# Performance work log

Measured on AMD Instinct MI355X. Metric: run time of the kernel, lower is better.

## Reference

```python
import jax, jax.numpy as jnp
import numpy as np

C, H, W = 3, 224, 224
P = 14  # patches per row
PS = H // P  # 16
PATCH_DIM = C * PS * PS  # 768
HIDDEN = 768


def patchify(images):
    # images: [n, c, h, w] -> [n, P*P, c*PS*PS], flatten order (c, ph, pw)
    n = images.shape[0]
    x = images.reshape(n, C, P, PS, P, PS)
    x = x.transpose(0, 2, 4, 1, 3, 5)  # [n, Pi, Pj, c, ps, ps]
    return x.reshape(n, P * P, PATCH_DIM)


def setup_inputs() -> dict:
    key = jax.random.key(0)
    k1, k2, k3 = jax.random.split(key, 3)
    images = jax.random.normal(k1, (128, C, H, W), dtype=jnp.float32)
    # nn.Linear(patch_embedding_dim, hidden_dim): weight [out, in], bias [out]
    bound = 1.0 / np.sqrt(PATCH_DIM)
    W_lin = jax.random.uniform(k2, (HIDDEN, PATCH_DIM), minval=-bound, maxval=bound, dtype=jnp.float32)
    b_lin = jax.random.uniform(k3, (HIDDEN,), minval=-bound, maxval=bound, dtype=jnp.float32)
    cls_token = jnp.ones((1, HIDDEN), dtype=jnp.float32)
    return {"images": images, "W_lin": W_lin, "b_lin": b_lin, "cls_token": cls_token}


def reference(images, W_lin, b_lin, cls_token):
    patches = patchify(images)                        # [n, 196, 768]
    hidden = jnp.einsum('npd,hd->nph', patches, W_lin) + b_lin  # [n, 196, H]
    n = images.shape[0]
    cls = jnp.broadcast_to(cls_token[None], (n, 1, HIDDEN))
    return jnp.concatenate([cls, hidden], axis=1)     # [n, 197, H]
```

## Files before the change

kernel.cpp:

```cpp
#include <hip/hip_runtime.h>
#include <cstdint>


#define PGRID 14
#define PSZ   16
#define CHN   3
#define IMGW  224
#define KDIM  768
#define NDIM  768
#define NPATCH 196

typedef short bf16x8 __attribute__((ext_vector_type(8)));
typedef short short8v __attribute__((ext_vector_type(8)));
typedef float f32x4  __attribute__((ext_vector_type(4)));

__device__ __forceinline__ short bf16rne(float f) {
    uint32_t u = __builtin_bit_cast(uint32_t, f);
    u += 0x7FFFu + ((u >> 16) & 1u);
    return (short)(u >> 16);
}

__device__ __forceinline__ short8v cvt8(float4 v0, float4 v1) {
    short8v s;
    s[0] = bf16rne(v0.x); s[1] = bf16rne(v0.y); s[2] = bf16rne(v0.z); s[3] = bf16rne(v0.w);
    s[4] = bf16rne(v1.x); s[5] = bf16rne(v1.y); s[6] = bf16rne(v1.z); s[7] = bf16rne(v1.w);
    return s;
}

__device__ __forceinline__ void gload_lds16(const void* g, void* l) {
    __builtin_amdgcn_global_load_lds(
        (const __attribute__((address_space(1))) unsigned int*)g,
        (__attribute__((address_space(3))) unsigned int*)l, 16, 0, 0);
}

__global__ __launch_bounds__(256) void prep_patch(
    const float* __restrict__ img, short* __restrict__ A, int M)
{
    int t = blockIdx.x * 256 + threadIdx.x;
    if (t >= M * 96) return;
    int m  = t / 96;
    int k8 = t - m * 96;
    int k  = k8 * 8;
    int c  = k >> 8;
    int ph = (k >> 4) & 15;
    int pw = k & 15;
    int im = m / NPATCH;
    int p  = m - im * NPATCH;
    int Pi = p / PGRID;
    int Pj = p - Pi * PGRID;
    const float* src = img + (((long)(im * CHN + c) * IMGW + Pi * PSZ + ph) * IMGW + Pj * PSZ + pw);
    float4 v0 = *(const float4*)src;
    float4 v1 = *(const float4*)(src + 4);
    *(short8v*)(A + (long)m * KDIM + k) = cvt8(v0, v1);
}

__global__ __launch_bounds__(256) void prep_small(
    const float* __restrict__ Wl, const float* __restrict__ cls,
    short* __restrict__ Wb, float* __restrict__ out, int n_img)
{
    int t = blockIdx.x * 256 + threadIdx.x;
    const int WCH = KDIM * NDIM / 8;
    if (t < WCH) {
        float4 v0 = *(const float4*)(Wl + (long)t * 8);
        float4 v1 = *(const float4*)(Wl + (long)t * 8 + 4);
        *(short8v*)(Wb + (long)t * 8) = cvt8(v0, v1);
    } else {
        int u = t - WCH;
        if (u < n_img * 96) {
            int im = u / 96;
            int k8 = u - im * 96;
            float4 v0 = *(const float4*)(cls + k8 * 8);
            float4 v1 = *(const float4*)(cls + k8 * 8 + 4);
            float* dst = out + (long)im * 197 * NDIM + k8 * 8;
            *(float4*)dst = v0;
            *(float4*)(dst + 4) = v1;
        }
    }
}

__global__ __launch_bounds__(256) void vit_gemm2(
    const short* __restrict__ A, const short* __restrict__ B,
    const float* __restrict__ bias, float* __restrict__ out, int M)
{
    __shared__ short As[128 * 64];
    __shared__ short Bs[128 * 64];

    const int tid = threadIdx.x;
    const int m0 = blockIdx.y * 128;
    const int n0 = blockIdx.x * 128;
    const int wave = tid >> 6;
    const int lane = tid & 63;

    const int srow = tid >> 3;
    const int sk   = (tid & 7) ^ (srow & 7);
    const long abase = (long)(m0 + srow) * KDIM + sk * 8;
    const long bbase = (long)(n0 + srow) * KDIM + sk * 8;
    char* AsB = (char*)As;
    char* BsB = (char*)Bs;
    const int ldsw = wave * 1024;

    const int wm = (wave & 1) * 64;
    const int wn = (wave >> 1) * 64;
    const int wq = lane >> 4;
    const int lr = lane & 15;
    const int blk0 = ((wq)     ^ (lr & 7)) * 8;
    const int blk1 = ((wq + 4) ^ (lr & 7)) * 8;

    f32x4 acc[4][4] = {};

    for (int kk = 0; kk < KDIM; kk += 64) {
        #pragma unroll
        for (int j = 0; j < 4; ++j) {
            gload_lds16(A + abase + (long)j * 32 * KDIM + kk, AsB + j * 4096 + ldsw);
            gload_lds16(B + bbase + (long)j * 32 * KDIM + kk, BsB + j * 4096 + ldsw);
        }
        __syncthreads();

        #pragma unroll
        for (int ks = 0; ks < 2; ++ks) {
            const int blk = ks ? blk1 : blk0;
            bf16x8 a[4], b[4];
            #pragma unroll
            for (int i = 0; i < 4; ++i)
                a[i] = *(const bf16x8*)(&As[(wm + i * 16 + lr) * 64 + blk]);
            #pragma unroll
            for (int i = 0; i < 4; ++i)
                b[i] = *(const bf16x8*)(&Bs[(wn + i * 16 + lr) * 64 + blk]);
            #pragma unroll
            for (int i = 0; i < 4; ++i)
                #pragma unroll
                for (int j = 0; j < 4; ++j)
                    acc[i][j] = __builtin_amdgcn_mfma_f32_16x16x32_bf16(a[i], b[j], acc[i][j], 0, 0, 0);
        }
        __syncthreads();
    }

    float bv[4];
    #pragma unroll
    for (int j = 0; j < 4; ++j) bv[j] = bias[n0 + wn + j * 16 + lr];

    #pragma unroll
    for (int i = 0; i < 4; ++i) {
        #pragma unroll
        for (int r = 0; r < 4; ++r) {
            int gm = m0 + wm + i * 16 + wq * 4 + r;
            if (gm < M) {
                int im = gm / NPATCH;
                int p  = gm - im * NPATCH;
                long orow = ((long)im * 197 + 1 + p) * (long)NDIM;
                #pragma unroll
                for (int j = 0; j < 4; ++j)
                    out[orow + n0 + wn + j * 16 + lr] = acc[i][j][r] + bv[j];
            }
        }
    }
}

#define LDSTR 40
__global__ __launch_bounds__(256) void vit_gemm_fb(
    const float* __restrict__ img, const float* __restrict__ Wl,
    const float* __restrict__ bias, float* __restrict__ out, int n_img)
{
    const int M = n_img * NPATCH;
    __shared__ short As[128 * LDSTR];
    __shared__ short Bs[128 * LDSTR];
    const int tid = threadIdx.x;
    const int m0 = blockIdx.y * 128;
    const int n0 = blockIdx.x * 128;
    const int col4  = tid & 7;
    const int rbase = tid >> 3;
    long arow[4];
    for (int rr = 0; rr < 4; ++rr) {
        int m = m0 + rbase + rr * 32;
        int mm = (m < M) ? m : (M - 1);
        int im = mm / NPATCH;
        int p  = mm % NPATCH;
        int Pi = p / PGRID;
        int Pj = p % PGRID;
        arow[rr] = ((long)(im * CHN) * IMGW + Pi * PSZ) * IMGW + Pj * PSZ;
    }
    const int lane = tid & 63;
    const int wave = tid >> 6;
    const int wm = (wave & 1) * 64;
    const int wn = (wave >> 1) * 64;
    const int wq = lane >> 4;
    const int lr = lane & 15;
    f32x4 acc[4][4] = {};
    for (int k0 = 0; k0 < KDIM; k0 += 32) {
        {
            int k  = k0 + col4 * 4;
            int c  = k >> 8;
            int ph = (k >> 4) & 15;
            int pw = k & 15;
            long koff = (long)(c * IMGW + ph) * IMGW + pw;
            #pragma unroll
            for (int rr = 0; rr < 4; ++rr) {
                const float4 v = *(const float4*)(img + arow[rr] + koff);
                int row = rbase + rr * 32;
                short4 s;
                s.x = bf16rne(v.x); s.y = bf16rne(v.y);
                s.z = bf16rne(v.z); s.w = bf16rne(v.w);
                *(short4*)(&As[row * LDSTR + col4 * 4]) = s;
            }
        }
        {
            int k = k0 + col4 * 4;
            #pragma unroll
            for (int rr = 0; rr < 4; ++rr) {
                int nrow = rbase + rr * 32;
                const float4 v = *(const float4*)(Wl + (long)(n0 + nrow) * KDIM + k);
                short4 s;
                s.x = bf16rne(v.x); s.y = bf16rne(v.y);
                s.z = bf16rne(v.z); s.w = bf16rne(v.w);
                *(short4*)(&Bs[nrow * LDSTR + col4 * 4]) = s;
            }
        }
        __syncthreads();
        bf16x8 a[4], b[4];
        #pragma unroll
        for (int i = 0; i < 4; ++i)
            a[i] = *(const bf16x8*)(&As[(wm + i * 16 + lr) * LDSTR + wq * 8]);
        #pragma unroll
        for (int i = 0; i < 4; ++i)
            b[i] = *(const bf16x8*)(&Bs[(wn + i * 16 + lr) * LDSTR + wq * 8]);
        #pragma unroll
        for (int i = 0; i < 4; ++i)
            #pragma unroll
            for (int j = 0; j < 4; ++j)
                acc[i][j] = __builtin_amdgcn_mfma_f32_16x16x32_bf16(a[i], b[j], acc[i][j], 0, 0, 0);
        __syncthreads();
    }
    float bv[4];
    #pragma unroll
    for (int j = 0; j < 4; ++j) bv[j] = bias[n0 + wn + j * 16 + lr];
    #pragma unroll
    for (int i = 0; i < 4; ++i) {
        #pragma unroll
        for (int r = 0; r < 4; ++r) {
            int gm = m0 + wm + i * 16 + wq * 4 + r;
            if (gm < M) {
                int im = gm / NPATCH;
                int p  = gm % NPATCH;
                long orow = ((long)im * 197 + 1 + p) * (long)NDIM;
                #pragma unroll
                for (int j = 0; j < 4; ++j)
                    out[orow + n0 + wn + j * 16 + lr] = acc[i][j][r] + bv[j];
            }
        }
    }
}

__global__ __launch_bounds__(256) void cls_fill(
    const float* __restrict__ cls, float* __restrict__ out, int n_img)
{
    int i = blockIdx.x * 256 + threadIdx.x;
    if (i < n_img * NDIM) {
        int im = i / NDIM;
        int n  = i - im * NDIM;
        out[(long)im * 197 * NDIM + n] = cls[n];
    }
}

extern "C" void kernel_launch(void* const* d_in, const int* in_sizes, int n_in,
                              void* d_out, int out_size, void* d_ws, size_t ws_size,
                              hipStream_t stream) {
    const float* img  = (const float*)d_in[0];
    const float* Wl   = (const float*)d_in[1];
    const float* bias = (const float*)d_in[2];
    const float* cls  = (const float*)d_in[3];
    float* out = (float*)d_out;

    int n_img = in_sizes[0] / (CHN * IMGW * IMGW);
    int M = n_img * NPATCH;
    int mblocks = (M + 127) / 128;
    long Mpad = (long)mblocks * 128;

    size_t need = (size_t)(Mpad * KDIM + (long)KDIM * NDIM) * sizeof(short);
    if (ws_size >= need) {
        short* A_ws = (short*)d_ws;
        short* Wb   = A_ws + Mpad * KDIM;

        prep_patch<<<(M * 96 + 255) / 256, 256, 0, stream>>>(img, A_ws, M);
        int small_total = KDIM * NDIM / 8 + n_img * 96;
        prep_small<<<(small_total + 255) / 256, 256, 0, stream>>>(Wl, cls, Wb, out, n_img);

        dim3 grid(NDIM / 128, mblocks);
        vit_gemm2<<<grid, 256, 0, stream>>>(A_ws, Wb, bias, out, M);
    } else {
        dim3 grid(NDIM / 128, mblocks);
        vit_gemm_fb<<<grid, 256, 0, stream>>>(img, Wl, bias, out, n_img);
        int cls_elems = n_img * NDIM;
        cls_fill<<<(cls_elems + 255) / 256, 256, 0, stream>>>(cls, out, n_img);
    }
}
```

Baseline: 193.9 us.

## Register-prefetch GEMM tiles and remap blocks for XCD-local M-tile sharing

Replaces the direct global-to-LDS loads with register staging, so the next K-slice is fetched from global memory while MFMAs run on the current slice in LDS. Also switches to a 1D grid where each XCD (block index mod 8) gets whole M-groups across all six N tiles, aiming to improve L2 reuse of A tiles. This costs extra VGPRs for the prefetch registers and an LDS store pass. The grid is padded to a multiple of 8 groups, and the surplus blocks exit early.

After: 181.4 us. 6.4% less time.

```diff
diff --git a/kernel.cpp b/kernel.cpp
--- a/kernel.cpp
+++ b/kernel.cpp
@@ -25,12 +25,6 @@
     s[0] = bf16rne(v0.x); s[1] = bf16rne(v0.y); s[2] = bf16rne(v0.z); s[3] = bf16rne(v0.w);
     s[4] = bf16rne(v1.x); s[5] = bf16rne(v1.y); s[6] = bf16rne(v1.z); s[7] = bf16rne(v1.w);
     return s;
-}
-
-__device__ __forceinline__ void gload_lds16(const void* g, void* l) {
-    __builtin_amdgcn_global_load_lds(
-        (const __attribute__((address_space(1))) unsigned int*)g,
-        (__attribute__((address_space(3))) unsigned int*)l, 16, 0, 0);
 }
 
 __global__ __launch_bounds__(256) void prep_patch(
@@ -78,16 +72,27 @@
     }
 }
 
-__global__ __launch_bounds__(256) void vit_gemm2(
+__global__ __launch_bounds__(256) void vit_gemm3(
     const short* __restrict__ A, const short* __restrict__ B,
-    const float* __restrict__ bias, float* __restrict__ out, int M)
-{
+    const float* __restrict__ bias, float* __restrict__ out,
+    int M, int mgroups)
+{
+    {
+    }
+    const int bid = blockIdx.x;
+    const int xcd = bid & 7;
+    const int s   = bid >> 3;
+    const int gq  = s / 6;
+    const int j   = s - gq * 6;
+    const int g   = gq * 8 + xcd;
+    if (g >= mgroups) return;
+    const int m0 = g * 128;
+    const int n0 = j * 128;
+
     __shared__ short As[128 * 64];
     __shared__ short Bs[128 * 64];
 
     const int tid = threadIdx.x;
-    const int m0 = blockIdx.y * 128;
-    const int n0 = blockIdx.x * 128;
     const int wave = tid >> 6;
     const int lane = tid & 63;
 
@@ -95,9 +100,6 @@
     const int sk   = (tid & 7) ^ (srow & 7);
     const long abase = (long)(m0 + srow) * KDIM + sk * 8;
     const long bbase = (long)(n0 + srow) * KDIM + sk * 8;
-    char* AsB = (char*)As;
-    char* BsB = (char*)Bs;
-    const int ldsw = wave * 1024;
 
     const int wm = (wave & 1) * 64;
     const int wn = (wave >> 1) * 64;
@@ -107,14 +109,29 @@
     const int blk1 = ((wq + 4) ^ (lr & 7)) * 8;
 
     f32x4 acc[4][4] = {};
+    bf16x8 ra[4], rb[4];
+
+    #pragma unroll
+    for (int jj = 0; jj < 4; ++jj) {
+        ra[jj] = *(const bf16x8*)(A + abase + (long)jj * 32 * KDIM);
+        rb[jj] = *(const bf16x8*)(B + bbase + (long)jj * 32 * KDIM);
+    }
 
     for (int kk = 0; kk < KDIM; kk += 64) {
         #pragma unroll
-        for (int j = 0; j < 4; ++j) {
-            gload_lds16(A + abase + (long)j * 32 * KDIM + kk, AsB + j * 4096 + ldsw);
-            gload_lds16(B + bbase + (long)j * 32 * KDIM + kk, BsB + j * 4096 + ldsw);
+        for (int jj = 0; jj < 4; ++jj) {
+            *(bf16x8*)(&As[(jj * 256 + tid) * 8]) = ra[jj];
+            *(bf16x8*)(&Bs[(jj * 256 + tid) * 8]) = rb[jj];
         }
         __syncthreads();
+
+        if (kk + 64 < KDIM) {
+            #pragma unroll
+            for (int jj = 0; jj < 4; ++jj) {
+                ra[jj] = *(const bf16x8*)(A + abase + (long)jj * 32 * KDIM + kk + 64);
+                rb[jj] = *(const bf16x8*)(B + bbase + (long)jj * 32 * KDIM + kk + 64);
+            }
+        }
 
         #pragma unroll
         for (int ks = 0; ks < 2; ++ks) {
@@ -129,15 +146,15 @@
             #pragma unroll
             for (int i = 0; i < 4; ++i)
                 #pragma unroll
-                for (int j = 0; j < 4; ++j)
-                    acc[i][j] = __builtin_amdgcn_mfma_f32_16x16x32_bf16(a[i], b[j], acc[i][j], 0, 0, 0);
+                for (int jm = 0; jm < 4; ++jm)
+                    acc[i][jm] = __builtin_amdgcn_mfma_f32_16x16x32_bf16(a[i], b[jm], acc[i][jm], 0, 0, 0);
         }
         __syncthreads();
     }
 
     float bv[4];
     #pragma unroll
-    for (int j = 0; j < 4; ++j) bv[j] = bias[n0 + wn + j * 16 + lr];
+    for (int jm = 0; jm < 4; ++jm) bv[jm] = bias[n0 + wn + jm * 16 + lr];
 
     #pragma unroll
     for (int i = 0; i < 4; ++i) {
@@ -149,8 +166,8 @@
                 int p  = gm - im * NPATCH;
                 long orow = ((long)im * 197 + 1 + p) * (long)NDIM;
                 #pragma unroll
-                for (int j = 0; j < 4; ++j)
-                    out[orow + n0 + wn + j * 16 + lr] = acc[i][j][r] + bv[j];
+                for (int jm = 0; jm < 4; ++jm)
+                    out[orow + n0 + wn + jm * 16 + lr] = acc[i][jm][r] + bv[jm];
             }
         }
     }
@@ -272,8 +289,8 @@
 
     int n_img = in_sizes[0] / (CHN * IMGW * IMGW);
     int M = n_img * NPATCH;
-    int mblocks = (M + 127) / 128;
-    long Mpad = (long)mblocks * 128;
+    int mgroups = (M + 127) / 128;
+    long Mpad = (long)mgroups * 128;
 
     size_t need = (size_t)(Mpad * KDIM + (long)KDIM * NDIM) * sizeof(short);
     if (ws_size >= need) {
@@ -284,10 +301,11 @@
         int small_total = KDIM * NDIM / 8 + n_img * 96;
         prep_small<<<(small_total + 255) / 256, 256, 0, stream>>>(Wl, cls, Wb, out, n_img);
 
-        dim3 grid(NDIM / 128, mblocks);
-        vit_gemm2<<<grid, 256, 0, stream>>>(A_ws, Wb, bias, out, M);
+        int gpad = (mgroups + 7) & ~7;
+        int nblocks = gpad * 6;
+        vit_gemm3<<<nblocks, 256, 0, stream>>>(A_ws, Wb, bias, out, M, mgroups);
     } else {
-        dim3 grid(NDIM / 128, mblocks);
+        dim3 grid(NDIM / 128, mgroups);
         vit_gemm_fb<<<grid, 256, 0, stream>>>(img, Wl, bias, out, n_img);
         int cls_elems = n_img * NDIM;
         cls_fill<<<(cls_elems + 255) / 256, 256, 0, stream>>>(cls, out, n_img);
```
